# Performance work log

Hardware: AMD Instinct MI355X
Metric: run time of the kernel (lower is better)

## Reference

```python
import jax, jax.numpy as jnp
import numpy as np

K = 5  # kensize -> kernel is (2K+1) x (2K+1) = 11x11


def _box_kernels(k):
    r = k
    s = 2 * r + 1
    M13 = np.concatenate([np.ones([r + 1, s]), np.zeros([r, s])], axis=0)  # top half (y1)
    M23 = np.concatenate([np.zeros([r, s]), np.ones([r + 1, s])], axis=0)  # bottom half (y2)
    M11 = np.concatenate([np.ones([s, r + 1]), np.zeros([s, r])], axis=1)  # left half (x1)
    M21 = np.concatenate([np.zeros([s, r]), np.ones([s, r + 1])], axis=1)  # right half (x2)
    to = lambda m: jnp.asarray(m, dtype=jnp.float32).reshape(1, 1, s, s)  # OIHW
    return to(M11), to(M21), to(M13), to(M23)


def setup_inputs() -> dict:
    key = jax.random.key(0)
    x = jax.random.uniform(key, (64, 1, 512, 512), dtype=jnp.float32)
    wx1, wx2, wy1, wy2 = _box_kernels(K)
    return {"x": x, "wx1": wx1, "wx2": wx2, "wy1": wy1, "wy2": wy2}


def _conv(x, w):
    return jax.lax.conv_general_dilated(
        x, w, window_strides=(1, 1), padding="VALID",
        dimension_numbers=("NCHW", "OIHW", "NCHW"))


def reference(x, wx1, wx2, wy1, wy2):
    # reflect-pad by K on H and W, then shift by 0.01 so box sums are > 0
    xp = jnp.pad(x, ((0, 0), (0, 0), (K, K), (K, K)), mode="reflect") + 0.01
    gx1 = _conv(xp, wx1)
    gx2 = _conv(xp, wx2)
    gy1 = _conv(xp, wy1)
    gy2 = _conv(xp, wy2)
    gx = jnp.log(gx1 / gx2)
    gy = jnp.log(gy1 / gy2)
    # L2 norm over the stacked (gx, gy) pair -> [B,1,H,W]
    return jnp.sqrt(gx * gx + gy * gy)
```

## Files before the change

kernel.cpp:

```cpp
#include <hip/hip_runtime.h>
#include <hip/hip_fp16.h>


#define N   512
#define TW  64
#define TH  32
#define SH  88
#define LN2 0.69314718056f

typedef __fp16 h2  __attribute__((ext_vector_type(2)));
typedef __fp16 h4v __attribute__((ext_vector_type(4)));
typedef __fp16 h8v __attribute__((ext_vector_type(8)));

__device__ __forceinline__ float2 f2add(float2 a, float2 b){ return make_float2(a.x+b.x, a.y+b.y); }
__device__ __forceinline__ float2 f2sub(float2 a, float2 b){ return make_float2(a.x-b.x, a.y-b.y); }

__device__ __forceinline__ void load20(const __half* __restrict__ arr, int base, float* __restrict__ t) {
    h8v a = *(const h8v*)(arr + base);
    h8v b = *(const h8v*)(arr + base + 8);
    h4v c = *(const h4v*)(arr + base + 16);
    #pragma unroll
    for (int j = 0; j < 8; ++j) t[j]     = (float)a[j];
    #pragma unroll
    for (int j = 0; j < 8; ++j) t[8 + j] = (float)b[j];
    #pragma unroll
    for (int j = 0; j < 4; ++j) t[16 + j] = (float)c[j];
}

__global__ __launch_bounds__(256, 6) void boxlog_kernel(
    const float* __restrict__ x, float* __restrict__ out)
{
    __shared__ __align__(16) __half topA [TH*SH];
    __shared__ __align__(16) __half botA [TH*SH];
    __shared__ __align__(16) __half fullA[TH*SH];

    const int tid = threadIdx.x;
    const int wg  = blockIdx.x;
    const int sw  = (wg & 7) * 1024 + (wg >> 3);
    const int bz  = sw >> 7;
    const int rem = sw & 127;
    const int by  = rem >> 3;
    const int bx  = rem & 7;
    const int X0 = bx * TW, Y0 = by * TH;
    const float* __restrict__ xb   = x   + (size_t)bz * ((size_t)N * N);
    float* __restrict__       outb = out + (size_t)bz * ((size_t)N * N);

    if (tid < 152) {
        const int rg = tid / 38;
        const int ch = tid - rg * 38;
        const int r0 = rg * 8;
        const int gc = X0 - 6 + 2 * ch;

        auto run = [&](auto loadrow) {
            float2 t[18];
            #pragma unroll
            for (int j = 0; j < 11; ++j) t[j] = loadrow(j);
            float2 tp = f2add(f2add(f2add(t[0],t[1]), f2add(t[2],t[3])), f2add(t[4],t[5]));
            float2 bt = f2add(f2add(f2add(t[5],t[6]), f2add(t[7],t[8])), f2add(t[9],t[10]));
            {
                float2 fu = f2sub(f2add(tp, bt), t[5]);
                const int b = r0 * SH + 2 * ch;
                *(h2*)&topA [b] = __builtin_amdgcn_cvt_pkrtz(tp.x + 0.06f, tp.y + 0.06f);
                *(h2*)&botA [b] = __builtin_amdgcn_cvt_pkrtz(bt.x + 0.06f, bt.y + 0.06f);
                *(h2*)&fullA[b] = __builtin_amdgcn_cvt_pkrtz(fu.x + 0.11f, fu.y + 0.11f);
            }
            #pragma unroll
            for (int k = 1; k < 8; ++k) {
                t[k+10] = loadrow(k + 10);
                tp = f2sub(f2add(tp, t[k+5]),  t[k-1]);
                bt = f2sub(f2add(bt, t[k+10]), t[k+4]);
                float2 fu = f2sub(f2add(tp, bt), t[k+5]);
                const int b = (r0 + k) * SH + 2 * ch;
                *(h2*)&topA [b] = __builtin_amdgcn_cvt_pkrtz(tp.x + 0.06f, tp.y + 0.06f);
                *(h2*)&botA [b] = __builtin_amdgcn_cvt_pkrtz(bt.x + 0.06f, bt.y + 0.06f);
                *(h2*)&fullA[b] = __builtin_amdgcn_cvt_pkrtz(fu.x + 0.11f, fu.y + 0.11f);
            }
        };

        if (by >= 1 && by <= 14 && bx >= 1 && bx <= 6) {
            run([&](int j) {
                return *(const float2*)(xb + (size_t)(Y0 - 5 + r0 + j) * N + gc);
            });
        } else {
            const bool vec = (gc >= 0) && (gc <= N - 2);
            run([&](int j) {
                int gr = Y0 - 5 + r0 + j;
                gr = gr < 0 ? -gr : (gr > N-1 ? 2*(N-1) - gr : gr);
                const float* rowp = xb + (size_t)gr * N;
                if (vec) return *(const float2*)(rowp + gc);
                int c0 = gc, c1 = gc + 1;
                c0 = c0 < 0 ? -c0 : (c0 > N-1 ? 2*(N-1) - c0 : c0);
                c1 = c1 < 0 ? -c1 : (c1 > N-1 ? 2*(N-1) - c1 : c1);
                return make_float2(rowp[c0], rowp[c1]);
            });
        }
    }
    __syncthreads();

    const int tx = tid & 7;
    const int ty = tid >> 3;
    const int base = ty * SH + 8 * tx;

    float gy1[8], ly[8];
    {
        float t[20];
        load20(topA, base, t);
        float g = ((t[1]+t[2])+(t[3]+t[4]))+((t[5]+t[6])+(t[7]+t[8]))+((t[9]+t[10])+t[11]);
        gy1[0] = g;
        #pragma unroll
        for (int p = 1; p < 8; ++p) { g += t[p+11] - t[p]; gy1[p] = g; }
    }
    {
        float t[20];
        load20(botA, base, t);
        float g = ((t[1]+t[2])+(t[3]+t[4]))+((t[5]+t[6])+(t[7]+t[8]))+((t[9]+t[10])+t[11]);
        ly[0] = __builtin_amdgcn_logf(gy1[0]) - __builtin_amdgcn_logf(g);
        #pragma unroll
        for (int p = 1; p < 8; ++p) {
            g += t[p+11] - t[p];
            ly[p] = __builtin_amdgcn_logf(gy1[p]) - __builtin_amdgcn_logf(g);
        }
    }
    {
        float t[20];
        load20(fullA, base, t);
        float g1 = ((t[1]+t[2])+(t[3]+t[4]))+(t[5]+t[6]);
        float g2 = ((t[6]+t[7])+(t[8]+t[9]))+(t[10]+t[11]);
        float r8[8];
        #pragma unroll
        for (int p = 0; p < 8; ++p) {
            if (p) {
                g1 += t[p+6]  - t[p];
                g2 += t[p+11] - t[p+5];
            }
            float lx = __builtin_amdgcn_logf(g1) - __builtin_amdgcn_logf(g2);
            r8[p] = LN2 * __builtin_amdgcn_sqrtf(lx*lx + ly[p]*ly[p]);
        }
        float* op = outb + (size_t)(Y0 + ty) * N + X0 + tx * 8;
        *(float4*)op       = make_float4(r8[0], r8[1], r8[2], r8[3]);
        *(float4*)(op + 4) = make_float4(r8[4], r8[5], r8[6], r8[7]);
    }
}

extern "C" void kernel_launch(void* const* d_in, const int* in_sizes, int n_in,
                              void* d_out, int out_size, void* d_ws, size_t ws_size,
                              hipStream_t stream) {
    const float* x = (const float*)d_in[0];
    float* out = (float*)d_out;
    dim3 grid(8 * 16 * 64);
    dim3 block(256);
    boxlog_kernel<<<grid, block, 0, stream>>>(x, out);
}
```

Measured before the change: 36.33 us.

## Use 64x64 tiles and derive top/bottom sums from one shared 6-row sum array

Each tile grows from 64x32 to 64x64, which halves the grid and lowers the fraction of halo rows re-read per tile. The separate top and bottom vertical-sum arrays are replaced by one 6-row sliding sum array with 69 rows. The bottom sum is then read from that array at a 5-row offset, which cuts shared-memory writes and the vertical-sum arithmetic. Each thread computes two output rows, and 228 threads run the column pass with uneven per-group row counts. The trade-off is fewer blocks in flight and more per-thread work, with shared memory rising to about 23 KB per block.

```diff
diff --git a/kernel.cpp b/kernel.cpp
--- a/kernel.cpp
+++ b/kernel.cpp
@@ -3,8 +3,6 @@
 
 
 #define N   512
-#define TW  64
-#define TH  32
 #define SH  88
 #define LN2 0.69314718056f
 
@@ -20,9 +18,9 @@
     h8v b = *(const h8v*)(arr + base + 8);
     h4v c = *(const h4v*)(arr + base + 16);
     #pragma unroll
-    for (int j = 0; j < 8; ++j) t[j]     = (float)a[j];
+    for (int j = 0; j < 8; ++j) t[j]      = (float)a[j];
     #pragma unroll
-    for (int j = 0; j < 8; ++j) t[8 + j] = (float)b[j];
+    for (int j = 0; j < 8; ++j) t[8 + j]  = (float)b[j];
     #pragma unroll
     for (int j = 0; j < 4; ++j) t[16 + j] = (float)c[j];
 }
@@ -30,61 +28,64 @@
 __global__ __launch_bounds__(256, 6) void boxlog_kernel(
     const float* __restrict__ x, float* __restrict__ out)
 {
-    __shared__ __align__(16) __half topA [TH*SH];
-    __shared__ __align__(16) __half botA [TH*SH];
-    __shared__ __align__(16) __half fullA[TH*SH];
+    __shared__ __align__(16) __half S6A [69*SH];
+    __shared__ __align__(16) __half fulA[64*SH];
 
     const int tid = threadIdx.x;
     const int wg  = blockIdx.x;
-    const int sw  = (wg & 7) * 1024 + (wg >> 3);
-    const int bz  = sw >> 7;
-    const int rem = sw & 127;
+    const int sw  = (wg & 7) * 512 + (wg >> 3);
+    const int bz  = sw >> 6;
+    const int rem = sw & 63;
     const int by  = rem >> 3;
     const int bx  = rem & 7;
-    const int X0 = bx * TW, Y0 = by * TH;
+    const int X0 = bx * 64, Y0 = by * 64;
     const float* __restrict__ xb   = x   + (size_t)bz * ((size_t)N * N);
     float* __restrict__       outb = out + (size_t)bz * ((size_t)N * N);
 
-    if (tid < 152) {
+    if (tid < 228) {
         const int rg = tid / 38;
         const int ch = tid - rg * 38;
-        const int r0 = rg * 8;
+        const int f0 = rg * 11;
         const int gc = X0 - 6 + 2 * ch;
 
-        auto run = [&](auto loadrow) {
-            float2 t[18];
+        auto body = [&](auto loadrow, auto NF, auto NS) {
+            constexpr int nf = decltype(NF)::value;
+            constexpr int ns = decltype(NS)::value;
+            float2 t[21];
             #pragma unroll
             for (int j = 0; j < 11; ++j) t[j] = loadrow(j);
-            float2 tp = f2add(f2add(f2add(t[0],t[1]), f2add(t[2],t[3])), f2add(t[4],t[5]));
-            float2 bt = f2add(f2add(f2add(t[5],t[6]), f2add(t[7],t[8])), f2add(t[9],t[10]));
+            float2 lo = f2add(f2add(f2add(t[0],t[1]), f2add(t[2],t[3])), f2add(t[4],t[5]));
+            float2 hi = f2add(f2add(f2add(t[5],t[6]), f2add(t[7],t[8])), f2add(t[9],t[10]));
             {
-                float2 fu = f2sub(f2add(tp, bt), t[5]);
-                const int b = r0 * SH + 2 * ch;
-                *(h2*)&topA [b] = __builtin_amdgcn_cvt_pkrtz(tp.x + 0.06f, tp.y + 0.06f);
-                *(h2*)&botA [b] = __builtin_amdgcn_cvt_pkrtz(bt.x + 0.06f, bt.y + 0.06f);
-                *(h2*)&fullA[b] = __builtin_amdgcn_cvt_pkrtz(fu.x + 0.11f, fu.y + 0.11f);
+                const int b = f0 * SH + 2 * ch;
+                float2 fu = f2sub(f2add(lo, hi), t[5]);
+                *(h2*)&S6A [b] = __builtin_amdgcn_cvt_pkrtz(lo.x + 0.06f, lo.y + 0.06f);
+                *(h2*)&fulA[b] = __builtin_amdgcn_cvt_pkrtz(fu.x + 0.11f, fu.y + 0.11f);
             }
             #pragma unroll
-            for (int k = 1; k < 8; ++k) {
-                t[k+10] = loadrow(k + 10);
-                tp = f2sub(f2add(tp, t[k+5]),  t[k-1]);
-                bt = f2sub(f2add(bt, t[k+10]), t[k+4]);
-                float2 fu = f2sub(f2add(tp, bt), t[k+5]);
-                const int b = (r0 + k) * SH + 2 * ch;
-                *(h2*)&topA [b] = __builtin_amdgcn_cvt_pkrtz(tp.x + 0.06f, tp.y + 0.06f);
-                *(h2*)&botA [b] = __builtin_amdgcn_cvt_pkrtz(bt.x + 0.06f, bt.y + 0.06f);
-                *(h2*)&fullA[b] = __builtin_amdgcn_cvt_pkrtz(fu.x + 0.11f, fu.y + 0.11f);
+            for (int k = 1; k < ns; ++k) {
+                if (k < nf) t[k+10] = loadrow(k + 10);
+                lo = f2sub(f2add(lo, t[k+5]), t[k-1]);
+                const int b = (f0 + k) * SH + 2 * ch;
+                *(h2*)&S6A[b] = __builtin_amdgcn_cvt_pkrtz(lo.x + 0.06f, lo.y + 0.06f);
+                if (k < nf) {
+                    hi = f2sub(f2add(hi, t[k+10]), t[k+4]);
+                    float2 fu = f2sub(f2add(lo, hi), t[k+5]);
+                    *(h2*)&fulA[b] = __builtin_amdgcn_cvt_pkrtz(fu.x + 0.11f, fu.y + 0.11f);
+                }
             }
         };
 
-        if (by >= 1 && by <= 14 && bx >= 1 && bx <= 6) {
-            run([&](int j) {
-                return *(const float2*)(xb + (size_t)(Y0 - 5 + r0 + j) * N + gc);
-            });
+        if (by >= 1 && by <= 6 && bx >= 1 && bx <= 6) {
+            auto lr = [&](int j) {
+                return *(const float2*)(xb + (size_t)(Y0 - 5 + f0 + j) * N + gc);
+            };
+            if (rg < 5) body(lr, std::integral_constant<int,11>{}, std::integral_constant<int,11>{});
+            else        body(lr, std::integral_constant<int, 9>{}, std::integral_constant<int,14>{});
         } else {
             const bool vec = (gc >= 0) && (gc <= N - 2);
-            run([&](int j) {
-                int gr = Y0 - 5 + r0 + j;
+            auto lr = [&](int j) {
+                int gr = Y0 - 5 + f0 + j;
                 gr = gr < 0 ? -gr : (gr > N-1 ? 2*(N-1) - gr : gr);
                 const float* rowp = xb + (size_t)gr * N;
                 if (vec) return *(const float2*)(rowp + gc);
@@ -92,53 +93,59 @@
                 c0 = c0 < 0 ? -c0 : (c0 > N-1 ? 2*(N-1) - c0 : c0);
                 c1 = c1 < 0 ? -c1 : (c1 > N-1 ? 2*(N-1) - c1 : c1);
                 return make_float2(rowp[c0], rowp[c1]);
-            });
+            };
+            if (rg < 5) body(lr, std::integral_constant<int,11>{}, std::integral_constant<int,11>{});
+            else        body(lr, std::integral_constant<int, 9>{}, std::integral_constant<int,14>{});
         }
     }
     __syncthreads();
 
     const int tx = tid & 7;
     const int ty = tid >> 3;
-    const int base = ty * SH + 8 * tx;
+    #pragma unroll
+    for (int s = 0; s < 2; ++s) {
+        const int row  = ty + 32 * s;
+        const int base = row * SH + 8 * tx;
 
-    float gy1[8], ly[8];
-    {
-        float t[20];
-        load20(topA, base, t);
-        float g = ((t[1]+t[2])+(t[3]+t[4]))+((t[5]+t[6])+(t[7]+t[8]))+((t[9]+t[10])+t[11]);
-        gy1[0] = g;
-        #pragma unroll
-        for (int p = 1; p < 8; ++p) { g += t[p+11] - t[p]; gy1[p] = g; }
-    }
-    {
-        float t[20];
-        load20(botA, base, t);
-        float g = ((t[1]+t[2])+(t[3]+t[4]))+((t[5]+t[6])+(t[7]+t[8]))+((t[9]+t[10])+t[11]);
-        ly[0] = __builtin_amdgcn_logf(gy1[0]) - __builtin_amdgcn_logf(g);
-        #pragma unroll
-        for (int p = 1; p < 8; ++p) {
-            g += t[p+11] - t[p];
-            ly[p] = __builtin_amdgcn_logf(gy1[p]) - __builtin_amdgcn_logf(g);
+        float gy1[8], ly[8];
+        {
+            float t[20];
+            load20(S6A, base, t);
+            float g = ((t[1]+t[2])+(t[3]+t[4]))+((t[5]+t[6])+(t[7]+t[8]))+((t[9]+t[10])+t[11]);
+            gy1[0] = g;
+            #pragma unroll
+            for (int p = 1; p < 8; ++p) { g += t[p+11] - t[p]; gy1[p] = g; }
         }
-    }
-    {
-        float t[20];
-        load20(fullA, base, t);
-        float g1 = ((t[1]+t[2])+(t[3]+t[4]))+(t[5]+t[6]);
-        float g2 = ((t[6]+t[7])+(t[8]+t[9]))+(t[10]+t[11]);
-        float r8[8];
-        #pragma unroll
-        for (int p = 0; p < 8; ++p) {
-            if (p) {
-                g1 += t[p+6]  - t[p];
-                g2 += t[p+11] - t[p+5];
+        {
+            float t[20];
+            load20(S6A, base + 5*SH, t);
+            float g = ((t[1]+t[2])+(t[3]+t[4]))+((t[5]+t[6])+(t[7]+t[8]))+((t[9]+t[10])+t[11]);
+            ly[0] = __builtin_amdgcn_logf(gy1[0]) - __builtin_amdgcn_logf(g);
+            #pragma unroll
+            for (int p = 1; p < 8; ++p) {
+                g += t[p+11] - t[p];
+                ly[p] = __builtin_amdgcn_logf(gy1[p]) - __builtin_amdgcn_logf(g);
             }
-            float lx = __builtin_amdgcn_logf(g1) - __builtin_amdgcn_logf(g2);
-            r8[p] = LN2 * __builtin_amdgcn_sqrtf(lx*lx + ly[p]*ly[p]);
         }
-        float* op = outb + (size_t)(Y0 + ty) * N + X0 + tx * 8;
-        *(float4*)op       = make_float4(r8[0], r8[1], r8[2], r8[3]);
-        *(float4*)(op + 4) = make_float4(r8[4], r8[5], r8[6], r8[7]);
+        {
+            float t[20];
+            load20(fulA, base, t);
+            float g1 = ((t[1]+t[2])+(t[3]+t[4]))+(t[5]+t[6]);
+            float g2 = ((t[6]+t[7])+(t[8]+t[9]))+(t[10]+t[11]);
+            float r8[8];
+            #pragma unroll
+            for (int p = 0; p < 8; ++p) {
+                if (p) {
+                    g1 += t[p+6]  - t[p];
+                    g2 += t[p+11] - t[p+5];
+                }
+                float lx = __builtin_amdgcn_logf(g1) - __builtin_amdgcn_logf(g2);
+                r8[p] = LN2 * __builtin_amdgcn_sqrtf(lx*lx + ly[p]*ly[p]);
+            }
+            float* op = outb + (size_t)(Y0 + row) * N + X0 + tx * 8;
+            *(float4*)op       = make_float4(r8[0], r8[1], r8[2], r8[3]);
+            *(float4*)(op + 4) = make_float4(r8[4], r8[5], r8[6], r8[7]);
+        }
     }
 }
 
@@ -147,7 +154,7 @@
                               hipStream_t stream) {
     const float* x = (const float*)d_in[0];
     float* out = (float*)d_out;
-    dim3 grid(8 * 16 * 64);
+    dim3 grid(8 * 8 * 64);
     dim3 block(256);
     boxlog_kernel<<<grid, block, 0, stream>>>(x, out);
 }
```

Result: faster. 34.87 us (-4.0%).
